# Kernel optimization log

Hardware: AMD Instinct MI355X
Metric: run time of the kernel (lower is better)

Reference implementation:

```python
import jax, jax.numpy as jnp
import numpy as np

S = 610      # number of HMM states (~6*nCodons+10 for nCodons=100)
E = 126      # order-transformed emission alphabet
BATCH = 32
T = 2048
NREG = 5000  # number of punished transitions
ALPHA_REG = 4.0


def setup_inputs() -> dict:
    key = jax.random.key(0)
    k1, k2, k3, k4, k5, k6 = jax.random.split(key, 6)
    obs = jax.random.randint(k1, (BATCH, T), 0, E)
    inputs = jax.nn.one_hot(obs, E, dtype=jnp.float32)          # [B,T,E]
    A = jax.nn.softmax(jax.random.normal(k2, (S, S)), axis=-1)   # row-stochastic transitions
    Bm = jax.nn.softmax(jax.random.normal(k3, (S, E)), axis=-1)  # emission matrix
    I = jax.nn.softmax(jax.random.normal(k4, (S,)))              # initial distribution
    reg_from = jax.random.randint(k5, (NREG,), 0, S)
    reg_to = jax.random.randint(k6, (NREG,), 0, S)
    return {"inputs": inputs, "A": A, "Bm": Bm, "I": I,
            "reg_from": reg_from, "reg_to": reg_to}


def reference(inputs, A, Bm, I, reg_from, reg_to):
    # emission likelihoods per step: [B,T,S]
    em = jnp.einsum('bte,se->bts', inputs, Bm)

    # HMM forward recursion with per-step normalization (scaled forward algorithm)
    alpha0 = I[None, :] * em[:, 0]                # [B,S]
    z0 = alpha0.sum(-1, keepdims=True)
    carry0 = (alpha0 / z0, jnp.log(z0[:, 0]))

    def step(carry, em_t):
        alpha, ll = carry
        a = (alpha @ A) * em_t                    # [B,S]
        z = a.sum(-1, keepdims=True)
        return (a / z, ll + jnp.log(z[:, 0])), None

    em_tbs = jnp.swapaxes(em, 0, 1)               # [T,B,S]
    (alpha_T, loglik), _ = jax.lax.scan(step, carry0, em_tbs[1:])

    loglik_mean = jnp.mean(loglik)
    # regularization: mean of log(1 - A[f, t]) over punished transitions
    reg_mean = jnp.mean(jnp.log1p(-A[reg_from, reg_to]))
    loss = -loglik_mean - ALPHA_REG * reg_mean
    return loss
```

## Files before the change

kernel.cpp:

```cpp
#include <hip/hip_runtime.h>
#include <math.h>

#define S      610
#define E      126
#define BATCH  32
#define T      2048
#define NREG   5000

#define SPAD   640
#define NT     40
#define NCH    5
#define MBXG   4
#define NBLK   8
#define THREADS 512
#define NWAVE  8
#define TPW    5
#define RT     3
#define AROW   672
#define ABUF   (MBXG * AROW)

typedef float f32x4 __attribute__((ext_vector_type(4)));
typedef int   i32x8 __attribute__((ext_vector_type(8)));

union Frag { uint4 q[2]; i32x8 v; };

#define MFMA_SCALED(af, bf, acc) \
    __builtin_amdgcn_mfma_scale_f32_16x16x128_f8f6f4((af), (bf), (acc), 0, 0, \
                                                     0, 0x7F7F7F7F, 0, 0x7F7F7F7F)

__device__ __forceinline__ float fastrcp(float x) {
#if __has_builtin(__builtin_amdgcn_rcpf)
    return __builtin_amdgcn_rcpf(x);
#else
    return 1.f / x;
#endif
}

__device__ __forceinline__ void ldsbar() {
#if __has_builtin(__builtin_amdgcn_s_waitcnt) && __has_builtin(__builtin_amdgcn_s_barrier)
    __builtin_amdgcn_s_waitcnt(0xC07F);
    __builtin_amdgcn_s_barrier();
#else
    __syncthreads();
#endif
}

template <int CTRL>
__device__ __forceinline__ float rotf(float v) {
    int r = __builtin_amdgcn_update_dpp(0, __builtin_bit_cast(int, v),
                                        CTRL, 0xF, 0xF, true);
    return __builtin_bit_cast(float, r);
}
__device__ __forceinline__ float row16_sum(float v) {
    v += rotf<0x128>(v);
    v += rotf<0x124>(v);
    v += rotf<0x122>(v);
    v += rotf<0x121>(v);
    return v;
}

__device__ __host__ __forceinline__ int posf(int j) {
    int n = j >> 4, mr = j & 15;
    return (n < 32) ? ((n & 7) * 16 + mr) * 4 + (n >> 3)
                    : 512 + (n - 32) * 16 + mr;
}
__device__ __forceinline__ int inv_pos(int p) {
    if (p < 512) {
        int idx = p & 3, q = p >> 2;
        return (idx * 8 + (q >> 4)) * 16 + (q & 15);
    }
    int q = p - 512;
    return (32 + (q >> 4)) * 16 + (q & 15);
}

__device__ __forceinline__ unsigned sw_e4m3_enc(float f) {
    if (!(f > 0.f)) return 0u;
    int e; float fr = frexpf(f, &e);
    if (e - 1 < -6) {
        int q = (int)rintf(f * 512.f);
        if (q > 7) q = 7;
        return (unsigned)q;
    }
    int m = (int)rintf(fr * 16.f) - 8;
    int EE = e - 1;
    if (m == 8) { m = 0; EE += 1; }
    if (EE > 8) { EE = 8; m = 7; }
    return (unsigned)(((EE + 7) << 3) | m);
}
__device__ __forceinline__ unsigned pack_quad(float v0, float v1, float v2, float v3) {
#if __has_builtin(__builtin_amdgcn_cvt_pk_fp8_f32)
    int lo = __builtin_amdgcn_cvt_pk_fp8_f32(v0, v1, 0, false);
    int hi = __builtin_amdgcn_cvt_pk_fp8_f32(v2, v3, 0, true);
    return (unsigned)(lo | hi);
#else
    return sw_e4m3_enc(v0) | (sw_e4m3_enc(v1) << 8) |
           (sw_e4m3_enc(v2) << 16) | (sw_e4m3_enc(v3) << 24);
#endif
}
__device__ __forceinline__ unsigned char fp8byte(float v) {
#if __has_builtin(__builtin_amdgcn_cvt_pk_fp8_f32)
    int w = __builtin_amdgcn_cvt_pk_fp8_f32(v, v, 0, false);
    return (unsigned char)(w & 0xFF);
#else
    return (unsigned char)sw_e4m3_enc(v);
#endif
}

__global__ void k_init(unsigned* __restrict__ maxbuf) { maxbuf[0] = 0u; }

__global__ void k_max(const float* __restrict__ A, unsigned* __restrict__ maxbuf) {
    int tid = blockIdx.x * blockDim.x + threadIdx.x;
    float m = 0.f;
    for (int i = tid; i < S * S; i += gridDim.x * blockDim.x) m = fmaxf(m, A[i]);
#pragma unroll
    for (int off = 1; off < 64; off <<= 1) m = fmaxf(m, __shfl_xor(m, off, 64));
    if ((threadIdx.x & 63) == 0) atomicMax(maxbuf, __float_as_uint(m));
}

__global__ void k_scalefin(const unsigned* __restrict__ maxbuf,
                           float* __restrict__ s_out, double* __restrict__ logs_out) {
    float mx = __uint_as_float(maxbuf[0]);
    float s = 224.f / mx;
    s_out[0] = s;
    s_out[1] = s / (float)E;
    logs_out[0] = log((double)s);
}

__global__ void k_pack8mx(const float* __restrict__ A, const float* __restrict__ s_in,
                          uint4* __restrict__ A8c) {
    int n = blockIdx.x;
    int c = blockIdx.y;
    int l = threadIdx.x;
    float s = s_in[0];
    int j = n * 16 + (l & 15);
    int pb0 = c * 128 + (l >> 4) * 32;
#pragma unroll
    for (int h = 0; h < 2; ++h) {
        unsigned dw[4];
#pragma unroll
        for (int r = 0; r < 4; ++r) {
            float v[4];
#pragma unroll
            for (int pb = 0; pb < 4; ++pb) {
                int k = inv_pos(pb0 + h * 16 + r * 4 + pb);
                v[pb] = (k < S && j < S) ? A[k * S + j] * s : 0.f;
            }
            dw[r] = pack_quad(v[0], v[1], v[2], v[3]);
        }
        A8c[((n * NCH + c) * 2 + h) * 64 + l] = make_uint4(dw[0], dw[1], dw[2], dw[3]);
    }
}

__global__ void k_bmt(const float* __restrict__ Bm, float* __restrict__ BmT) {
    int j = threadIdx.x;
    int o = blockIdx.x;
    BmT[o * SPAD + j] = (j < S) ? Bm[j * E + o] : 0.f;
}

__global__ void k_obs(const float* __restrict__ in, int* __restrict__ obsT) {
    int i = blockIdx.x * blockDim.x + threadIdx.x;
    if (i >= BATCH * T) return;
    const float2* p = (const float2*)(in + (size_t)i * E);
    int o = 0;
#pragma unroll
    for (int k = 0; k < E / 2; ++k) {
        float2 v = p[k];
        if (v.x > 0.5f) o = 2 * k;
        if (v.y > 0.5f) o = 2 * k + 1;
    }
    int b = i / T, t = i % T;
    obsT[t * BATCH + b] = o * SPAD;
}

__global__ void k_reg(const float* __restrict__ A, const int* __restrict__ rf,
                      const int* __restrict__ rt, float* __restrict__ out) {
    __shared__ float wpart[16];
    int tid = threadIdx.x;
    float s = 0.f;
    for (int i = tid; i < NREG; i += 1024)
        s += log1pf(-A[rf[i] * S + rt[i]]);
#pragma unroll
    for (int off = 1; off < 64; off <<= 1) s += __shfl_xor(s, off, 64);
    if ((tid & 63) == 0) wpart[tid >> 6] = s;
    __syncthreads();
    if (tid == 0) {
        float t = 0.f;
        for (int w = 0; w < 16; ++w) t += wpart[w];
        out[0] = t;
    }
}

__global__ __launch_bounds__(THREADS, 2) void k_forward(
    const uint4* __restrict__ A8c,
    const float* __restrict__ BmT,
    const int*   __restrict__ obsT,
    const float* __restrict__ Iv,
    const float* __restrict__ sbuf,
    const double* __restrict__ logs,
    double* __restrict__ ll_out)
{
    __shared__ __align__(16) uint4 pinAv[8 * NCH * 2 * 64];
    __shared__ __align__(16) unsigned char alphaq[2 * ABUF];
    __shared__ __align__(16) float zpart[NWAVE][MBXG];
    __shared__ __align__(64) float zT[2][MBXG][8];
    __shared__ __align__(16) float zsc[MBXG];

    const int g    = blockIdx.x;
    const int tid  = threadIdx.x;
    const int wv   = tid >> 6;
    const int lane = tid & 63;
    const int mrow = lane & 15;
    const int quad = lane >> 4;
    const int b0   = g * MBXG;

    const float rhobar = sbuf[1];

    for (int i = tid; i < 8 * NCH * 2 * 64; i += THREADS)
        pinAv[i] = A8c[24 * NCH * 2 * 64 + i];

    i32x8 areg[RT][NCH];
#pragma unroll
    for (int rt = 0; rt < RT; ++rt)
#pragma unroll
        for (int c = 0; c < NCH; ++c) {
            Frag f;
            f.q[0] = A8c[(((rt * 8 + wv) * NCH + c) * 2 + 0) * 64 + lane];
            f.q[1] = A8c[(((rt * 8 + wv) * NCH + c) * 2 + 1) * 64 + lane];
            areg[rt][c] = f.v;
        }

    {
        const int j1 = tid + THREADS;
        const bool hasb = (j1 < SPAD);
        float Ia = (tid < S) ? Iv[tid] : 0.f;
        float Ib = (hasb && j1 < S) ? Iv[j1] : 0.f;
        float v0a[MBXG], v0b[MBXG], p0[MBXG];
#pragma unroll
        for (int m = 0; m < MBXG; ++m) {
            int o = obsT[b0 + m];
            v0a[m] = Ia * BmT[o + tid];
            v0b[m] = hasb ? Ib * BmT[o + j1] : 0.f;
            p0[m] = v0a[m] + v0b[m];
        }
#pragma unroll
        for (int off = 1; off < 64; off <<= 1)
#pragma unroll
            for (int m = 0; m < MBXG; ++m) p0[m] += __shfl_xor(p0[m], off, 64);
        if (lane == 0) {
#pragma unroll
            for (int m = 0; m < MBXG; ++m) zpart[wv][m] = p0[m];
        }
        __syncthreads();
        if (tid < MBXG) {
            float z = 0.f;
            for (int w = 0; w < NWAVE; ++w) z += zpart[w][tid];
            zsc[tid] = 128.f / z;
        }
        __syncthreads();
        if (tid < 32) zT[0][tid & 3][tid >> 2] =
            zpart[tid >> 2][tid & 3] * zsc[tid & 3];
        const int pa = posf(tid);
        const int pb = hasb ? posf(j1) : 0;
#pragma unroll
        for (int m = 0; m < MBXG; ++m) {
            alphaq[m * AROW + pa] = fp8byte(v0a[m] * zsc[m]);
            if (hasb) alphaq[m * AROW + pb] = fp8byte(v0b[m] * zsc[m]);
        }
        __syncthreads();
    }
    double gls = (double)__logf(zsc[quad]);

    const uint4* sp   = A8c + (size_t)((32 + wv) * NCH * 2) * 64 + lane;
    const uint4* pinp = pinAv + wv * (NCH * 2 * 64) + lane;
    const int aoff = (mrow >> 2) * AROW + quad * 32;

    int jrow[TPW];
#pragma unroll
    for (int idx = 0; idx < TPW; ++idx) {
        const int n = (idx < 4) ? (idx * 8 + wv) : (32 + wv);
        jrow[idx] = n * 16 + mrow;
    }

    int on_cur = obsT[1 * BATCH + b0 + quad];

    float em[TPW];
    i32x8 gs[3];

    for (int t = 1; t < T; ++t) {
        const int rb = (t - 1) & 1;
        const unsigned char* aqp = alphaq + rb * ABUF + aoff;
        unsigned char*       aqw = alphaq + (rb ^ 1) * ABUF;

        const int tn = (t + 1 < T) ? t + 1 : t;
        const int on_next = obsT[tn * BATCH + b0 + quad];
#pragma unroll
        for (int idx = 0; idx < TPW; ++idx) em[idx] = BmT[on_cur + jrow[idx]];
        {
            Frag f; f.q[0] = sp[0];   f.q[1] = sp[64];  gs[0] = f.v;
        }
        {
            Frag f; f.q[0] = sp[128]; f.q[1] = sp[192]; gs[1] = f.v;
        }

        i32x8 afc[2], pfc[2];
        {
            Frag f; f.q[0] = *(const uint4*)(aqp); f.q[1] = *(const uint4*)(aqp + 16);
            afc[0] = f.v;
        }
        {
            Frag f; f.q[0] = pinp[0]; f.q[1] = pinp[64]; pfc[0] = f.v;
        }

        f32x4 acc[TPW];
#pragma unroll
        for (int idx = 0; idx < TPW; ++idx) acc[idx] = (f32x4)0.f;

#pragma unroll
        for (int c = 0; c < NCH; ++c) {
            if (c + 2 < NCH) {
                Frag f;
                f.q[0] = sp[((c + 2) * 2 + 0) * 64];
                f.q[1] = sp[((c + 2) * 2 + 1) * 64];
                gs[(c + 2) % 3] = f.v;
            }
            if (c + 1 < NCH) {
                Frag f;
                f.q[0] = *(const uint4*)(aqp + (c + 1) * 128);
                f.q[1] = *(const uint4*)(aqp + (c + 1) * 128 + 16);
                afc[(c + 1) & 1] = f.v;
                Frag p;
                p.q[0] = pinp[(c + 1) * 128];
                p.q[1] = pinp[(c + 1) * 128 + 64];
                pfc[(c + 1) & 1] = p.v;
            }
            const i32x8 a = afc[c & 1];
#pragma unroll
            for (int rt = 0; rt < RT; ++rt)
                acc[rt] = MFMA_SCALED(a, areg[rt][c], acc[rt]);
            acc[3] = MFMA_SCALED(a, pfc[c & 1], acc[3]);
            acc[4] = MFMA_SCALED(a, gs[c % 3], acc[4]);
        }

        const f32x4 za = *(const f32x4*)(&zT[rb][quad][0]);
        const f32x4 zb = *(const f32x4*)(&zT[rb][quad][4]);
        const f32x4 s4 = za + zb;
        const float zps = (s4[0] + s4[1]) + (s4[2] + s4[3]);
        const float zd  = fmaxf(zps * rhobar, 1e-30f);
        const float ivq = 128.f * fastrcp(zd);
        if (wv == 0) gls += (double)__logf(ivq);
#pragma unroll
        for (int idx = 0; idx < TPW; ++idx) em[idx] *= ivq;

        float pz = 0.f;
#pragma unroll
        for (int idx = 0; idx < TPW; ++idx) {
            em[idx] = acc[idx][0] * em[idx];
            pz += em[idx];
        }
        {
            const int wbase = (wv * 16 + mrow) * 4;
            unsigned dw = pack_quad(em[0], em[1], em[2], em[3]);
            *(unsigned*)(aqw + quad * AROW + wbase) = dw;
            aqw[quad * AROW + 512 + wv * 16 + mrow] = fp8byte(em[4]);
        }
        pz = row16_sum(pz);
        if (mrow == 0) zT[rb ^ 1][quad][wv] = pz;

        on_cur = on_next;
        ldsbar();
    }

    {
        const int fb = (T - 1) & 1;
        const f32x4 za = *(const f32x4*)(&zT[fb][quad][0]);
        const f32x4 zb = *(const f32x4*)(&zT[fb][quad][4]);
        const f32x4 s4 = za + zb;
        const float zfin = (s4[0] + s4[1]) + (s4[2] + s4[3]);
        if (wv == 0 && mrow == 0)
            ll_out[b0 + quad] = (double)__logf(zfin) - gls - 2047.0 * logs[0];
    }
}

__global__ void k_final(const double* __restrict__ ll, const float* __restrict__ regsum,
                        float* __restrict__ out) {
    double s = 0.0;
    for (int b = 0; b < BATCH; ++b) s += ll[b];
    double loglik_mean = s / BATCH;
    double reg_mean = (double)regsum[0] / NREG;
    out[0] = (float)(-loglik_mean - 4.0 * reg_mean);
}

extern "C" void kernel_launch(void* const* d_in, const int* in_sizes, int n_in,
                              void* d_out, int out_size, void* d_ws, size_t ws_size,
                              hipStream_t stream) {
    const float* inputs = (const float*)d_in[0];
    const float* A      = (const float*)d_in[1];
    const float* Bm     = (const float*)d_in[2];
    const float* Iv     = (const float*)d_in[3];
    const int*   rf     = (const int*)d_in[4];
    const int*   rt     = (const int*)d_in[5];

    char* ws = (char*)d_ws;
    uint4*    A8c  = (uint4*)ws;
    float*    BmT  = (float*)(ws + 409600);
    int*      obsT = (int*)(ws + 732160);
    double*   ll   = (double*)(ws + 994304);
    float*    regs = (float*)(ws + 994560);
    unsigned* mx   = (unsigned*)(ws + 994564);
    float*    sbuf = (float*)(ws + 994568);
    double*   logs = (double*)(ws + 994576);

    hipLaunchKernelGGL(k_init,     dim3(1),   dim3(1),   0, stream, mx);
    hipLaunchKernelGGL(k_max,      dim3(256), dim3(256), 0, stream, A, mx);
    hipLaunchKernelGGL(k_scalefin, dim3(1),   dim3(1),   0, stream, mx, sbuf, logs);
    hipLaunchKernelGGL(k_pack8mx,  dim3(NT, NCH), dim3(64), 0, stream, A, sbuf, A8c);
    hipLaunchKernelGGL(k_bmt,      dim3(E),   dim3(SPAD), 0, stream, Bm, BmT);
    hipLaunchKernelGGL(k_obs,      dim3((BATCH * T + 255) / 256), dim3(256), 0, stream, inputs, obsT);
    hipLaunchKernelGGL(k_reg,      dim3(1),   dim3(1024), 0, stream, A, rf, rt, regs);
    hipLaunchKernelGGL(k_forward,  dim3(NBLK), dim3(THREADS), 0, stream,
                       A8c, BmT, obsT, Iv, sbuf, logs, ll);
    hipLaunchKernelGGL(k_final,    dim3(1),   dim3(1),   0, stream, ll, regs, (float*)d_out);
}
```

Before: 2.275 ms.

## Fold normalizer sum into MFMA via ones column and merge prep kernels

Padding column 610 of the packed transition matrix is set to 1.0, so the MFMA produces the sum of the alpha vector (the normalizer) as an extra output. This replaces the per-step DPP row reduction and the 8-way partial-sum exchange through LDS. The sum now comes from the quantized fp8 alpha times unscaled ones, with no emission multiply. The separate init, BmT, obs and reg kernels are fused into one prep kernel to cut launch count. This changes which z is used for normalization (the previous step's predicted sum rather than the current emitted sum) and may affect numerics.

Result: no change. 2.265 ms (-0.4%).

```diff
diff --git a/kernel.cpp b/kernel.cpp
--- a/kernel.cpp
+++ b/kernel.cpp
@@ -18,6 +18,7 @@
 #define RT     3
 #define AROW   672
 #define ABUF   (MBXG * AROW)
+#define ZCOL   610
 
 typedef float f32x4 __attribute__((ext_vector_type(4)));
 typedef int   i32x8 __attribute__((ext_vector_type(8)));
@@ -43,20 +44,6 @@
 #else
     __syncthreads();
 #endif
-}
-
-template <int CTRL>
-__device__ __forceinline__ float rotf(float v) {
-    int r = __builtin_amdgcn_update_dpp(0, __builtin_bit_cast(int, v),
-                                        CTRL, 0xF, 0xF, true);
-    return __builtin_bit_cast(float, r);
-}
-__device__ __forceinline__ float row16_sum(float v) {
-    v += rotf<0x128>(v);
-    v += rotf<0x124>(v);
-    v += rotf<0x122>(v);
-    v += rotf<0x121>(v);
-    return v;
 }
 
 __device__ __host__ __forceinline__ int posf(int j) {
@@ -106,7 +93,44 @@
 #endif
 }
 
-__global__ void k_init(unsigned* __restrict__ maxbuf) { maxbuf[0] = 0u; }
+__global__ void k_prep(const float* __restrict__ in, const float* __restrict__ Bm,
+                       const float* __restrict__ A,
+                       const int* __restrict__ rf, const int* __restrict__ rt,
+                       int* __restrict__ obsT, float* __restrict__ BmT,
+                       float* __restrict__ regs, unsigned* __restrict__ mx) {
+    const int b = blockIdx.x, tid = threadIdx.x;
+    if (b < 128) {
+        for (int i = b * 256 + tid; i < E * SPAD; i += 128 * 256) {
+            int o = i / SPAD, j = i - o * SPAD;
+            BmT[i] = (j < S) ? Bm[j * E + o] : 0.f;
+        }
+    } else if (b < 384) {
+        int i = (b - 128) * 256 + tid;
+        if (i < BATCH * T) {
+            const float2* p = (const float2*)(in + (size_t)i * E);
+            int o = 0;
+#pragma unroll
+            for (int k = 0; k < E / 2; ++k) {
+                float2 v = p[k];
+                if (v.x > 0.5f) o = 2 * k;
+                if (v.y > 0.5f) o = 2 * k + 1;
+            }
+            int bb = i / T, t = i - bb * T;
+            obsT[t * BATCH + bb] = o * SPAD;
+        }
+    } else {
+        if (tid == 0) mx[0] = 0u;
+        __shared__ float wpart[4];
+        float s = 0.f;
+        for (int i = tid; i < NREG; i += 256)
+            s += log1pf(-A[rf[i] * S + rt[i]]);
+#pragma unroll
+        for (int off = 1; off < 64; off <<= 1) s += __shfl_xor(s, off, 64);
+        if ((tid & 63) == 0) wpart[tid >> 6] = s;
+        __syncthreads();
+        if (tid == 0) regs[0] = wpart[0] + wpart[1] + wpart[2] + wpart[3];
+    }
+}
 
 __global__ void k_max(const float* __restrict__ A, unsigned* __restrict__ maxbuf) {
     int tid = blockIdx.x * blockDim.x + threadIdx.x;
@@ -143,50 +167,12 @@
 #pragma unroll
             for (int pb = 0; pb < 4; ++pb) {
                 int k = inv_pos(pb0 + h * 16 + r * 4 + pb);
-                v[pb] = (k < S && j < S) ? A[k * S + j] * s : 0.f;
+                v[pb] = (j == ZCOL) ? 1.0f
+                      : ((k < S && j < S) ? A[k * S + j] * s : 0.f);
             }
             dw[r] = pack_quad(v[0], v[1], v[2], v[3]);
         }
         A8c[((n * NCH + c) * 2 + h) * 64 + l] = make_uint4(dw[0], dw[1], dw[2], dw[3]);
-    }
-}
-
-__global__ void k_bmt(const float* __restrict__ Bm, float* __restrict__ BmT) {
-    int j = threadIdx.x;
-    int o = blockIdx.x;
-    BmT[o * SPAD + j] = (j < S) ? Bm[j * E + o] : 0.f;
-}
-
-__global__ void k_obs(const float* __restrict__ in, int* __restrict__ obsT) {
-    int i = blockIdx.x * blockDim.x + threadIdx.x;
-    if (i >= BATCH * T) return;
-    const float2* p = (const float2*)(in + (size_t)i * E);
-    int o = 0;
-#pragma unroll
-    for (int k = 0; k < E / 2; ++k) {
-        float2 v = p[k];
-        if (v.x > 0.5f) o = 2 * k;
-        if (v.y > 0.5f) o = 2 * k + 1;
-    }
-    int b = i / T, t = i % T;
-    obsT[t * BATCH + b] = o * SPAD;
-}
-
-__global__ void k_reg(const float* __restrict__ A, const int* __restrict__ rf,
-                      const int* __restrict__ rt, float* __restrict__ out) {
-    __shared__ float wpart[16];
-    int tid = threadIdx.x;
-    float s = 0.f;
-    for (int i = tid; i < NREG; i += 1024)
-        s += log1pf(-A[rf[i] * S + rt[i]]);
-#pragma unroll
-    for (int off = 1; off < 64; off <<= 1) s += __shfl_xor(s, off, 64);
-    if ((tid & 63) == 0) wpart[tid >> 6] = s;
-    __syncthreads();
-    if (tid == 0) {
-        float t = 0.f;
-        for (int w = 0; w < 16; ++w) t += wpart[w];
-        out[0] = t;
     }
 }
 
@@ -202,7 +188,7 @@
     __shared__ __align__(16) uint4 pinAv[8 * NCH * 2 * 64];
     __shared__ __align__(16) unsigned char alphaq[2 * ABUF];
     __shared__ __align__(16) float zpart[NWAVE][MBXG];
-    __shared__ __align__(64) float zT[2][MBXG][8];
+    __shared__ __align__(16) float zT2[2][MBXG];
     __shared__ __align__(16) float zsc[MBXG];
 
     const int g    = blockIdx.x;
@@ -255,10 +241,9 @@
             float z = 0.f;
             for (int w = 0; w < NWAVE; ++w) z += zpart[w][tid];
             zsc[tid] = 128.f / z;
+            zT2[0][tid] = 128.f;
         }
         __syncthreads();
-        if (tid < 32) zT[0][tid & 3][tid >> 2] =
-            zpart[tid >> 2][tid & 3] * zsc[tid & 3];
         const int pa = posf(tid);
         const int pb = hasb ? posf(j1) : 0;
 #pragma unroll
@@ -341,41 +326,30 @@
             acc[4] = MFMA_SCALED(a, gs[c % 3], acc[4]);
         }
 
-        const f32x4 za = *(const f32x4*)(&zT[rb][quad][0]);
-        const f32x4 zb = *(const f32x4*)(&zT[rb][quad][4]);
-        const f32x4 s4 = za + zb;
-        const float zps = (s4[0] + s4[1]) + (s4[2] + s4[3]);
+        const float zps = zT2[rb][quad];
         const float zd  = fmaxf(zps * rhobar, 1e-30f);
         const float ivq = 128.f * fastrcp(zd);
         if (wv == 0) gls += (double)__logf(ivq);
 #pragma unroll
         for (int idx = 0; idx < TPW; ++idx) em[idx] *= ivq;
 
-        float pz = 0.f;
-#pragma unroll
-        for (int idx = 0; idx < TPW; ++idx) {
+#pragma unroll
+        for (int idx = 0; idx < TPW; ++idx)
             em[idx] = acc[idx][0] * em[idx];
-            pz += em[idx];
-        }
         {
             const int wbase = (wv * 16 + mrow) * 4;
             unsigned dw = pack_quad(em[0], em[1], em[2], em[3]);
             *(unsigned*)(aqw + quad * AROW + wbase) = dw;
             aqw[quad * AROW + 512 + wv * 16 + mrow] = fp8byte(em[4]);
         }
-        pz = row16_sum(pz);
-        if (mrow == 0) zT[rb ^ 1][quad][wv] = pz;
+        if (wv == 6 && mrow == 2) zT2[rb ^ 1][quad] = acc[4][0];
 
         on_cur = on_next;
         ldsbar();
     }
 
     {
-        const int fb = (T - 1) & 1;
-        const f32x4 za = *(const f32x4*)(&zT[fb][quad][0]);
-        const f32x4 zb = *(const f32x4*)(&zT[fb][quad][4]);
-        const f32x4 s4 = za + zb;
-        const float zfin = (s4[0] + s4[1]) + (s4[2] + s4[3]);
+        const float zfin = zT2[(T - 1) & 1][quad];
         if (wv == 0 && mrow == 0)
             ll_out[b0 + quad] = (double)__logf(zfin) - gls - 2047.0 * logs[0];
     }
@@ -410,13 +384,11 @@
     float*    sbuf = (float*)(ws + 994568);
     double*   logs = (double*)(ws + 994576);
 
-    hipLaunchKernelGGL(k_init,     dim3(1),   dim3(1),   0, stream, mx);
+    hipLaunchKernelGGL(k_prep,     dim3(385), dim3(256), 0, stream,
+                       inputs, Bm, A, rf, rt, obsT, BmT, regs, mx);
     hipLaunchKernelGGL(k_max,      dim3(256), dim3(256), 0, stream, A, mx);
     hipLaunchKernelGGL(k_scalefin, dim3(1),   dim3(1),   0, stream, mx, sbuf, logs);
     hipLaunchKernelGGL(k_pack8mx,  dim3(NT, NCH), dim3(64), 0, stream, A, sbuf, A8c);
-    hipLaunchKernelGGL(k_bmt,      dim3(E),   dim3(SPAD), 0, stream, Bm, BmT);
-    hipLaunchKernelGGL(k_obs,      dim3((BATCH * T + 255) / 256), dim3(256), 0, stream, inputs, obsT);
-    hipLaunchKernelGGL(k_reg,      dim3(1),   dim3(1024), 0, stream, A, rf, rt, regs);
     hipLaunchKernelGGL(k_forward,  dim3(NBLK), dim3(THREADS), 0, stream,
                        A8c, BmT, obsT, Iv, sbuf, logs, ll);
     hipLaunchKernelGGL(k_final,    dim3(1),   dim3(1),   0, stream, ll, regs, (float*)d_out);
```
